# Kernel tuning notes

Hardware: AMD Instinct MI355X
Metric: run time of the kernel (lower is better)

## Reference

```python
import jax, jax.numpy as jnp
import numpy as np

EMBED_DIM = 1024
NUM_HEADS = 16
HEAD_DIM = EMBED_DIM // NUM_HEADS
MAX_SEQ_LEN = 2048
ROPE_BASE = 10000.0


def _rope_tables(head_dim, max_seq_len, base):
    # inv_freq: (head_dim/2,)
    inv_freq = 1.0 / base ** (jnp.arange(0, head_dim, 2, dtype=jnp.float32) / head_dim)
    positions = jnp.arange(max_seq_len, dtype=jnp.float32)
    angles = positions[:, None] * inv_freq[None, :]  # (S, head_dim/2)
    # Original repeat_interleaves then slices [0::2], which recovers per-pair angles.
    return jnp.cos(angles), jnp.sin(angles)


def _apply_rope(x, cos, sin):
    # x: (B, H, S, D); cos/sin: (S, D/2)
    x_even = x[..., 0::2]
    x_odd = x[..., 1::2]
    c = cos[None, None, :, :]
    s = sin[None, None, :, :]
    x_even_rot = x_even * c - x_odd * s
    x_odd_rot = x_even * s + x_odd * c
    # interleave back: stack pairs on last dim and flatten
    x_rot = jnp.stack([x_even_rot, x_odd_rot], axis=-1)
    return x_rot.reshape(x.shape)


def setup_inputs() -> dict:
    key = jax.random.key(0)
    k1, k2, k3, k4 = jax.random.split(key, 4)
    B, S, E = 2, 2048, EMBED_DIM
    x = jax.random.normal(k1, (B, S, E), dtype=jnp.float32)
    bound_in = np.sqrt(6.0 / (3 * E + E)).astype(np.float32)
    in_proj_weight = jax.random.uniform(k2, (3 * E, E), minval=-bound_in, maxval=bound_in, dtype=jnp.float32)
    in_proj_bias = jnp.zeros((3 * E,), dtype=jnp.float32)
    bound_out = np.sqrt(6.0 / (E + E)).astype(np.float32)
    out_proj_weight = jax.random.uniform(k3, (E, E), minval=-bound_out, maxval=bound_out, dtype=jnp.float32)
    out_proj_bias = jnp.zeros((E,), dtype=jnp.float32)
    return {
        "query": x,
        "key": x,
        "value": x,
        "in_proj_weight": in_proj_weight,
        "in_proj_bias": in_proj_bias,
        "out_proj_weight": out_proj_weight,
        "out_proj_bias": out_proj_bias,
    }


def reference(query, key, value, in_proj_weight, in_proj_bias, out_proj_weight, out_proj_bias):
    B, S, E = query.shape
    H, D = NUM_HEADS, HEAD_DIM
    cos, sin = _rope_tables(D, MAX_SEQ_LEN, ROPE_BASE)
    cos, sin = cos[:S], sin[:S]

    # fused QKV projection (note: original applies in_proj to `query` only — self-attention)
    qkv = query @ in_proj_weight.T + in_proj_bias  # (B, S, 3E)
    q, k, v = jnp.split(qkv, 3, axis=-1)
    q = q.reshape(B, S, H, D).transpose(0, 2, 1, 3)  # (B, H, S, D)
    k = k.reshape(B, S, H, D).transpose(0, 2, 1, 3)
    v = v.reshape(B, S, H, D).transpose(0, 2, 1, 3)

    q = _apply_rope(q, cos, sin)
    k = _apply_rope(k, cos, sin)

    scale = 1.0 / np.sqrt(D).astype(np.float32)
    scores = jnp.einsum("bhqd,bhkd->bhqk", q, k) * scale
    attn = jax.nn.softmax(scores, axis=-1)
    out = jnp.einsum("bhqk,bhkd->bhqd", attn, v)  # (B, H, S, D)
    out = out.transpose(0, 2, 1, 3).reshape(B, S, E)
    return out @ out_proj_weight.T + out_proj_bias
```

## Files before the change

kernel.cpp:

```cpp
#include <hip/hip_runtime.h>
#include <hip/hip_bf16.h>
#include <cstdint>
#include <cstddef>

typedef __bf16 bf16;
typedef bf16 bf16x2 __attribute__((ext_vector_type(2)));
typedef bf16 bf16x4 __attribute__((ext_vector_type(4)));
typedef bf16 bf16x8 __attribute__((ext_vector_type(8)));
typedef float f32x4 __attribute__((ext_vector_type(4)));
typedef float f32x16 __attribute__((ext_vector_type(16)));

#define SEQ 2048
#define EMB 1024
#define NH 16
#define HD 64
#define BSZ 2
#define MROWS (BSZ*SEQ)

__device__ __forceinline__ void gload_lds16(const void* g, void* lds) {
  __builtin_amdgcn_global_load_lds((__attribute__((address_space(1))) void*)g,
                                   (__attribute__((address_space(3))) void*)lds,
                                   16, 0, 0);
}

__global__ void prep_kernel(const float* __restrict__ s0, bf16* __restrict__ d0, int n0_4,
                            const float* __restrict__ s1, bf16* __restrict__ d1, int n1_4,
                            const float* __restrict__ s2, bf16* __restrict__ d2, int n2_4,
                            float* __restrict__ cosT, float* __restrict__ sinT) {
  int j = blockIdx.x * blockDim.x + threadIdx.x;
  const float* s; bf16* d;
  if (j < n0_4) { s = s0; d = d0; }
  else {
    int j1 = j - n0_4;
    if (j1 < n1_4) { s = s1; d = d1; j = j1; }
    else {
      int j2 = j1 - n1_4;
      if (j2 < n2_4) { s = s2; d = d2; j = j2; }
      else {
        int idx = j2 - n2_4;
        if (idx >= SEQ * 32) return;
        int ss = idx >> 5, jj = idx & 31;
        float ex = (2.0f * (float)jj) / 64.0f;
        float inv = 1.0f / powf(10000.0f, ex);
        float ang = (float)ss * inv;
        cosT[idx] = cosf(ang);
        sinT[idx] = sinf(ang);
        return;
      }
    }
  }
  const float4 v = reinterpret_cast<const float4*>(s)[j];
  bf16x4 o;
  o[0] = (bf16)v.x; o[1] = (bf16)v.y; o[2] = (bf16)v.z; o[3] = (bf16)v.w;
  reinterpret_cast<bf16x4*>(d)[j] = o;
}

template<int EPI, int BM>
__launch_bounds__(256)
__global__ void gemm_bt(const bf16* __restrict__ A, const bf16* __restrict__ B,
                        const float* __restrict__ bias,
                        float* __restrict__ Cf,
                        bf16* __restrict__ qb, bf16* __restrict__ kb, bf16* __restrict__ vt,
                        const float* __restrict__ cosT, const float* __restrict__ sinT,
                        int Ndim, int Kdim) {
  constexpr int MREP = BM / 32;
  __shared__ __align__(16) bf16 Alds[2][BM * 32];
  __shared__ __align__(16) bf16 Blds[2][128 * 32];
  const int tid = threadIdx.x;
  const int wave = tid >> 6, lane = tid & 63;
  const int wr = wave >> 1, wc = wave & 1;
  const int bm = blockIdx.x * BM, bn = blockIdx.y * 128;

  f32x4 acc[MREP][4] = {};

  const int srow = lane >> 2;
  const int scol = (lane & 3) * 8;

  for (int kt = 0; kt < Kdim; kt += 64) {
#pragma unroll
    for (int hf = 0; hf < 2; hf++) {
      char* aldsb = (char*)Alds[hf];
      char* bldsb = (char*)Blds[hf];
      const int kc = kt + hf * 32;
#pragma unroll
      for (int c = 0; c < BM / 64; c++)
        gload_lds16(A + (size_t)(bm + (wave + 4 * c) * 16 + srow) * Kdim + kc + scol,
                    aldsb + wave * 1024 + c * 4096);
      gload_lds16(B + (size_t)(bn + wave * 16 + srow) * Kdim + kc + scol, bldsb + wave * 1024);
      gload_lds16(B + (size_t)(bn + (wave + 4) * 16 + srow) * Kdim + kc + scol, bldsb + wave * 1024 + 4096);
    }
    __syncthreads();
#pragma unroll
    for (int hf = 0; hf < 2; hf++) {
      bf16x8 af[MREP], bfr[4];
#pragma unroll
      for (int m = 0; m < MREP; m++)
        af[m] = *reinterpret_cast<const bf16x8*>(Alds[hf] + (wr * (BM / 2) + m * 16 + (lane & 15)) * 32 + (lane >> 4) * 8);
#pragma unroll
      for (int n = 0; n < 4; n++)
        bfr[n] = *reinterpret_cast<const bf16x8*>(Blds[hf] + (wc * 64 + n * 16 + (lane & 15)) * 32 + (lane >> 4) * 8);
#pragma unroll
      for (int m = 0; m < MREP; m++)
#pragma unroll
        for (int n = 0; n < 4; n++)
          acc[m][n] = __builtin_amdgcn_mfma_f32_16x16x32_bf16(af[m], bfr[n], acc[m][n], 0, 0, 0);
    }
    __syncthreads();
  }

  if (EPI == 1 && bn >= 2 * EMB) {
#pragma unroll
    for (int m = 0; m < MREP; m++) {
#pragma unroll
      for (int n = 0; n < 4; n++) {
        const int col = bn + wc * 64 + n * 16 + (lane & 15);
        const int rem = col & 1023;
        const int h = rem >> 6, d = rem & 63;
        const int row0 = bm + wr * (BM / 2) + m * 16 + (lane >> 4) * 4;
        const int b = row0 >> 11, s0 = row0 & (SEQ - 1);
        const float bs = bias[col];
        bf16x4 o;
#pragma unroll
        for (int r = 0; r < 4; r++) o[r] = (bf16)(acc[m][n][r] + bs);
        *reinterpret_cast<bf16x4*>(vt + (((size_t)(b * NH + h) * HD) + d) * SEQ + s0) = o;
      }
    }
  } else {
#pragma unroll
    for (int m = 0; m < MREP; m++) {
#pragma unroll
      for (int n = 0; n < 4; n++) {
#pragma unroll
        for (int r = 0; r < 4; r++) {
          const int row = bm + wr * (BM / 2) + m * 16 + (lane >> 4) * 4 + r;
          const int col = bn + wc * 64 + n * 16 + (lane & 15);
          const float v = acc[m][n][r] + bias[col];
          if (EPI == 0) {
            Cf[(size_t)row * Ndim + col] = v;
          } else {
            const int b = row >> 11, s = row & (SEQ - 1);
            const int which = col >> 10, rem = col & 1023;
            const int h = rem >> 6, d = rem & 63;
            const float vp = __shfl_xor(v, 1, 64);
            const int jj = d >> 1;
            const float c = cosT[(s << 5) + jj], sn = sinT[(s << 5) + jj];
            float vr = (d & 1) ? (vp * sn + v * c) : (v * c - vp * sn);
            if (which == 0) {
              vr *= 0.125f;
              qb[(((size_t)(b * NH + h) * SEQ) + s) * HD + d] = (bf16)vr;
            } else {
              kb[(((size_t)(b * NH + h) * SEQ) + s) * HD + d] = (bf16)vr;
            }
          }
        }
      }
    }
  }
}

__device__ __forceinline__ unsigned pk2(float a, float b) {
  bf16x2 t; t[0] = (bf16)a; t[1] = (bf16)b;
  unsigned u; __builtin_memcpy(&u, &t, 4); return u;
}

#define KPITCH 144

#define STAGE_LOAD(KV0) do { \
  kr0 = *(const int4*)(Kb + (size_t)((KV0) + (gtid >> 3)) * HD + (gtid & 7) * 8); \
  kr1 = *(const int4*)(Kb + (size_t)((KV0) + 32 + (gtid >> 3)) * HD + (gtid & 7) * 8); \
  vr0 = *(const int4*)(Vb + (size_t)(gtid >> 3) * SEQ + (KV0) + (gtid & 7) * 8); \
  vr1 = *(const int4*)(Vb + (size_t)(32 + (gtid >> 3)) * SEQ + (KV0) + (gtid & 7) * 8); \
} while (0)

#define STAGE_WRITE(BUF) do { \
  *(int4*)(Klds[grp][BUF] + (gtid >> 3) * KPITCH + (gtid & 7) * 16) = kr0; \
  *(int4*)(Klds[grp][BUF] + ((gtid >> 3) + 32) * KPITCH + (gtid & 7) * 16) = kr1; \
  const int vo_ = ((gtid & 7) >> 1) * 32 + ((gtid & 7) & 1) * 8; \
  char* v0p_ = Vlds[grp][BUF] + (gtid >> 3) * KPITCH + vo_; \
  char* v1p_ = Vlds[grp][BUF] + ((gtid >> 3) + 32) * KPITCH + vo_; \
  *(int2*)(v0p_)      = make_int2(vr0.x, vr0.y); \
  *(int2*)(v0p_ + 16) = make_int2(vr0.z, vr0.w); \
  *(int2*)(v1p_)      = make_int2(vr1.x, vr1.y); \
  *(int2*)(v1p_ + 16) = make_int2(vr1.z, vr1.w); \
} while (0)

#define COMPUTE_TILE64(BUFI) do { \
  const char* kbp = Klds[grp][BUFI]; const char* vbp = Vlds[grp][BUFI]; \
  bf16x8 KF[2][4], VF[2][4]; \
  _Pragma("unroll") \
  for (int hh = 0; hh < 2; hh++) \
    _Pragma("unroll") \
    for (int dk = 0; dk < 4; dk++) \
      KF[hh][dk] = *reinterpret_cast<const bf16x8*>(kbp + (hh * 32 + ql) * KPITCH + dk * 32 + hi * 16); \
  _Pragma("unroll") \
  for (int hh = 0; hh < 2; hh++) \
    _Pragma("unroll") \
    for (int i = 0; i < 4; i++) \
      VF[hh][i] = *reinterpret_cast<const bf16x8*>(vbp + ((i >> 1) * 32 + ql) * KPITCH + hh * 64 + (i & 1) * 32 + hi * 16); \
  f32x16 s0 = {}, s1 = {}; \
  __builtin_amdgcn_s_setprio(1); \
  _Pragma("unroll") \
  for (int dk = 0; dk < 4; dk++) { \
    s0 = __builtin_amdgcn_mfma_f32_32x32x16_bf16(KF[0][dk], qf[dk], s0, 0, 0, 0); \
    s1 = __builtin_amdgcn_mfma_f32_32x32x16_bf16(KF[1][dk], qf[dk], s1, 0, 0, 0); \
  } \
  __builtin_amdgcn_s_setprio(0); \
  float p0[16], p1[16]; \
  _Pragma("unroll") \
  for (int r = 0; r < 16; r++) { p0[r] = __expf(s0[r] - 12.f); p1[r] = __expf(s1[r] - 12.f); } \
  _Pragma("unroll") \
  for (int r = 0; r < 16; r++) psum[r] += p0[r] + p1[r]; \
   \
  bf16x8 pf[2][2]; \
  { \
    unsigned w00[4] = { pk2(p0[0], p0[1]),  pk2(p0[2], p0[3]),   pk2(p0[4], p0[5]),   pk2(p0[6], p0[7]) }; \
    unsigned w01[4] = { pk2(p0[8], p0[9]),  pk2(p0[10], p0[11]), pk2(p0[12], p0[13]), pk2(p0[14], p0[15]) }; \
    unsigned w10[4] = { pk2(p1[0], p1[1]),  pk2(p1[2], p1[3]),   pk2(p1[4], p1[5]),   pk2(p1[6], p1[7]) }; \
    unsigned w11[4] = { pk2(p1[8], p1[9]),  pk2(p1[10], p1[11]), pk2(p1[12], p1[13]), pk2(p1[14], p1[15]) }; \
    __builtin_memcpy(&pf[0][0], w00, 16); \
    __builtin_memcpy(&pf[0][1], w01, 16); \
    __builtin_memcpy(&pf[1][0], w10, 16); \
    __builtin_memcpy(&pf[1][1], w11, 16); \
  } \
  __builtin_amdgcn_s_setprio(1); \
  _Pragma("unroll") \
  for (int hh = 0; hh < 2; hh++) { \
    oacc0 = __builtin_amdgcn_mfma_f32_32x32x16_bf16(VF[hh][0], pf[hh][0], oacc0, 0, 0, 0); \
    oacc0 = __builtin_amdgcn_mfma_f32_32x32x16_bf16(VF[hh][1], pf[hh][1], oacc0, 0, 0, 0); \
    oacc1 = __builtin_amdgcn_mfma_f32_32x32x16_bf16(VF[hh][2], pf[hh][0], oacc1, 0, 0, 0); \
    oacc1 = __builtin_amdgcn_mfma_f32_32x32x16_bf16(VF[hh][3], pf[hh][1], oacc1, 0, 0, 0); \
  } \
  __builtin_amdgcn_s_setprio(0); \
} while (0)

__launch_bounds__(512)
__global__ void attn_kernel(const bf16* __restrict__ qb, const bf16* __restrict__ kb,
                            const bf16* __restrict__ vt, bf16* __restrict__ ob) {
  const int bid = (blockIdx.x & 7) * 64 + (blockIdx.x >> 3);
  const int qblk = bid & 15;
  const int bh = bid >> 4;
  const int b = bh >> 4, h = bh & 15;
  const int tid = threadIdx.x;
  const int wave = tid >> 6;
  const int grp = wave >> 2;
  const int wsub = wave & 3;
  const int gtid = tid & 255;
  const int lane = tid & 63;
  const int q0 = qblk * 128 + wsub * 32;
  const int ql = lane & 31, hi = lane >> 5;

  __shared__ __align__(16) char Klds[2][2][64 * KPITCH];
  __shared__ __align__(16) char Vlds[2][2][64 * KPITCH];

  const bf16* Qb = qb + (size_t)bh * SEQ * HD;
  const bf16* Kb = kb + (size_t)bh * SEQ * HD + (size_t)grp * 1024 * HD;
  const bf16* Vb = vt + (size_t)bh * HD * SEQ + grp * 1024;

  bf16x8 qf[4];
#pragma unroll
  for (int dk = 0; dk < 4; dk++)
    qf[dk] = *reinterpret_cast<const bf16x8*>(Qb + (size_t)(q0 + ql) * HD + dk * 16 + hi * 8);

  f32x16 oacc0 = {}, oacc1 = {};
  float psum[16];
#pragma unroll
  for (int r = 0; r < 16; r++) psum[r] = 0.f;

  int4 kr0, kr1, vr0, vr1;
  STAGE_LOAD(0);
  STAGE_WRITE(0);
  __syncthreads();

  for (int t = 0; t < 16; ++t) {
    const int cur = t & 1;
    if (t < 15) STAGE_LOAD((t + 1) * 64);
    COMPUTE_TILE64(cur);
    if (t < 15) STAGE_WRITE(cur ^ 1);
    __syncthreads();
  }

#pragma unroll
  for (int r = 0; r < 8; r++) psum[r] += psum[r + 8];
#pragma unroll
  for (int r = 0; r < 4; r++) psum[r] += psum[r + 4];
  float lrun = (psum[0] + psum[1]) + (psum[2] + psum[3]);
  lrun += __shfl_xor(lrun, 32, 64);

  float* cb = (float*)(&Klds[0][0][0]);
  float* myb = cb + (wsub * 64 + lane) * 34;
  if (grp == 1) {
#pragma unroll
    for (int r = 0; r < 16; r++) { myb[r] = oacc0[r]; myb[16 + r] = oacc1[r]; }
    myb[32] = lrun;
  }
  __syncthreads();
  if (grp == 0) {
    const float inv = 1.0f / (lrun + myb[32]);
    const size_t orow = ((size_t)b * SEQ + q0 + ql) * EMB + h * HD;
#pragma unroll
    for (int r = 0; r < 16; r++) {
      const int d = (r & 3) + 8 * (r >> 2) + 4 * hi;
      ob[orow + d]      = (bf16)((oacc0[r] + myb[r]) * inv);
      ob[orow + 32 + d] = (bf16)((oacc1[r] + myb[16 + r]) * inv);
    }
  }
}

extern "C" void kernel_launch(void* const* d_in, const int* in_sizes, int n_in,
                              void* d_out, int out_size, void* d_ws, size_t ws_size,
                              hipStream_t stream) {
  const float* x    = (const float*)d_in[0];
  const float* Win  = (const float*)d_in[3];
  const float* bin  = (const float*)d_in[4];
  const float* Wout = (const float*)d_in[5];
  const float* bout = (const float*)d_in[6];
  float* out = (float*)d_out;

  char* p = (char*)d_ws;
  bf16* xb  = (bf16*)p; p += (size_t)MROWS * EMB * 2;
  bf16* wb  = (bf16*)p; p += (size_t)3 * EMB * EMB * 2;
  bf16* wob = (bf16*)p; p += (size_t)EMB * EMB * 2;
  bf16* qb  = (bf16*)p; p += (size_t)MROWS * EMB * 2;
  bf16* kb  = (bf16*)p; p += (size_t)MROWS * EMB * 2;
  bf16* vt  = (bf16*)p; p += (size_t)MROWS * EMB * 2;
  bf16* ob  = (bf16*)p; p += (size_t)MROWS * EMB * 2;
  float* cosT = (float*)p; p += (size_t)SEQ * 32 * 4;
  float* sinT = (float*)p; p += (size_t)SEQ * 32 * 4;

  const int n0 = MROWS * EMB / 4, n1 = 3 * EMB * EMB / 4, n2 = EMB * EMB / 4;
  const int ntot = n0 + n1 + n2 + SEQ * 32;
  prep_kernel<<<(ntot + 255) / 256, 256, 0, stream>>>(x, xb, n0, Win, wb, n1, Wout, wob, n2, cosT, sinT);

  gemm_bt<1, 128><<<dim3(MROWS / 128, 3 * EMB / 128), 256, 0, stream>>>(
      xb, wb, bin, nullptr, qb, kb, vt, cosT, sinT, 3 * EMB, EMB);
  attn_kernel<<<BSZ * NH * (SEQ / 128), 512, 0, stream>>>(qb, kb, vt, ob);
  gemm_bt<0, 64><<<dim3(MROWS / 64, EMB / 128), 256, 0, stream>>>(
      ob, wob, bout, out, nullptr, nullptr, nullptr, nullptr, nullptr, EMB, EMB);
}
```

Measured before the change: 131.9 us.

## Double-buffer GEMM LDS stages to overlap global loads with MFMA

Replaces the load-both-halves-then-compute loop in the GEMM kernel with a ping-pong pipeline over 32-wide K slices. The next slice's global-to-LDS loads are issued before the MFMAs on the current buffer. The aim is to hide global load latency behind compute. In exchange there is one barrier per 32-wide slice instead of per 64, and the correctness of the async global_load_lds relies on the barrier waiting for the loads to finish.

```diff
diff --git a/kernel.cpp b/kernel.cpp
--- a/kernel.cpp
+++ b/kernel.cpp
@@ -76,37 +76,38 @@
   const int srow = lane >> 2;
   const int scol = (lane & 3) * 8;
 
-  for (int kt = 0; kt < Kdim; kt += 64) {
-#pragma unroll
-    for (int hf = 0; hf < 2; hf++) {
-      char* aldsb = (char*)Alds[hf];
-      char* bldsb = (char*)Blds[hf];
-      const int kc = kt + hf * 32;
-#pragma unroll
-      for (int c = 0; c < BM / 64; c++)
-        gload_lds16(A + (size_t)(bm + (wave + 4 * c) * 16 + srow) * Kdim + kc + scol,
-                    aldsb + wave * 1024 + c * 4096);
-      gload_lds16(B + (size_t)(bn + wave * 16 + srow) * Kdim + kc + scol, bldsb + wave * 1024);
-      gload_lds16(B + (size_t)(bn + (wave + 4) * 16 + srow) * Kdim + kc + scol, bldsb + wave * 1024 + 4096);
-    }
+#define GSTAGE(BUF, KC) do { \
+  char* aldsb = (char*)Alds[BUF]; \
+  char* bldsb = (char*)Blds[BUF]; \
+  _Pragma("unroll") \
+  for (int c = 0; c < BM / 64; c++) \
+    gload_lds16(A + (size_t)(bm + (wave + 4 * c) * 16 + srow) * Kdim + (KC) + scol, \
+                aldsb + wave * 1024 + c * 4096); \
+  gload_lds16(B + (size_t)(bn + wave * 16 + srow) * Kdim + (KC) + scol, bldsb + wave * 1024); \
+  gload_lds16(B + (size_t)(bn + (wave + 4) * 16 + srow) * Kdim + (KC) + scol, bldsb + wave * 1024 + 4096); \
+} while (0)
+
+  GSTAGE(0, 0);
+  __syncthreads();
+
+  for (int kt = 0; kt < Kdim; kt += 32) {
+    const int cur = (kt >> 5) & 1;
+    if (kt + 32 < Kdim) GSTAGE(cur ^ 1, kt + 32);
+    bf16x8 af[MREP], bfr[4];
+#pragma unroll
+    for (int m = 0; m < MREP; m++)
+      af[m] = *reinterpret_cast<const bf16x8*>(Alds[cur] + (wr * (BM / 2) + m * 16 + (lane & 15)) * 32 + (lane >> 4) * 8);
+#pragma unroll
+    for (int n = 0; n < 4; n++)
+      bfr[n] = *reinterpret_cast<const bf16x8*>(Blds[cur] + (wc * 64 + n * 16 + (lane & 15)) * 32 + (lane >> 4) * 8);
+#pragma unroll
+    for (int m = 0; m < MREP; m++)
+#pragma unroll
+      for (int n = 0; n < 4; n++)
+        acc[m][n] = __builtin_amdgcn_mfma_f32_16x16x32_bf16(af[m], bfr[n], acc[m][n], 0, 0, 0);
     __syncthreads();
-#pragma unroll
-    for (int hf = 0; hf < 2; hf++) {
-      bf16x8 af[MREP], bfr[4];
-#pragma unroll
-      for (int m = 0; m < MREP; m++)
-        af[m] = *reinterpret_cast<const bf16x8*>(Alds[hf] + (wr * (BM / 2) + m * 16 + (lane & 15)) * 32 + (lane >> 4) * 8);
-#pragma unroll
-      for (int n = 0; n < 4; n++)
-        bfr[n] = *reinterpret_cast<const bf16x8*>(Blds[hf] + (wc * 64 + n * 16 + (lane & 15)) * 32 + (lane >> 4) * 8);
-#pragma unroll
-      for (int m = 0; m < MREP; m++)
-#pragma unroll
-        for (int n = 0; n < 4; n++)
-          acc[m][n] = __builtin_amdgcn_mfma_f32_16x16x32_bf16(af[m], bfr[n], acc[m][n], 0, 0, 0);
-    }
-    __syncthreads();
-  }
+  }
+#undef GSTAGE
 
   if (EPI == 1 && bn >= 2 * EMB) {
 #pragma unroll
```

Result: no change. 134.4 us (+1.9%).
